# Optimization experiments

Measured on AMD Instinct MI355X. Metric: run time of the kernel, lower is better.

## Reference

```python
import jax, jax.numpy as jnp
import numpy as np


def _assignment(rows, n_clusters, portion, dtype):
    # eye(n_clusters) repeat_interleaved `portion` times along rows, truncated to `rows`,
    # plus the same matrix rolled down by `portion` rows (overlapping assignment).
    s = (jnp.arange(rows)[:, None] // portion == jnp.arange(n_clusters)[None, :]).astype(dtype)
    return s + jnp.roll(s, portion, axis=0)


def _dense_gcn(x, adj, W, b):
    # PyG DenseGCNConv: set diag to 1 (self loops), symmetric deg^-1/2 normalization,
    # out = A_norm @ (x W) + b
    n = adj.shape[0]
    idx = jnp.arange(n)
    adj = adj.at[idx, idx].set(1.0)
    out = x @ W
    d = jnp.clip(jnp.sum(adj, axis=-1), 1.0, None) ** -0.5
    adj = d[:, None] * adj * d[None, :]
    return adj @ out + b


def setup_inputs() -> dict:
    key = jax.random.key(0)
    ks = jax.random.split(key, 8)
    N, D, H, O = 4096, 128, 128, 2
    x = jax.random.normal(ks[0], (N, D), dtype=jnp.float32)
    edge_index = jax.random.uniform(ks[1], (2, N, N), dtype=jnp.float32)  # [1] slice = dense adjacency
    ca1 = jax.random.normal(ks[2], (D, D), dtype=jnp.float32) * (1.414 / np.sqrt(D))  # xavier_normal gain 1.414
    W1 = jax.random.normal(ks[3], (D, H), dtype=jnp.float32) * 0.05
    b1 = jnp.zeros((H,), dtype=jnp.float32)
    W2 = jax.random.normal(ks[4], (H, H), dtype=jnp.float32) * 0.05
    b2 = jnp.zeros((H,), dtype=jnp.float32)
    Wlin = jax.random.normal(ks[5], (O, H), dtype=jnp.float32) * 0.05
    blin = jnp.zeros((O,), dtype=jnp.float32)
    return {"x": x, "edge_index": edge_index, "num_nodes1": 2048,
            "ca1": ca1, "W1": W1, "b1": b1, "W2": W2, "b2": b2,
            "Wlin": Wlin, "blin": blin}


def reference(x, edge_index, num_nodes1, ca1, W1, b1, W2, b2, Wlin, blin):
    N = x.shape[0]
    nearest = N + (N % 2)
    n1 = nearest // 2
    n2 = n1
    portion1 = -(-nearest // n1)  # ceil
    dt = x.dtype

    # level-1 overlapping assignment [N, n1]
    flat_s = _assignment(N, n1, portion1, dt)
    newadj = edge_index[1]
    x1 = flat_s.T @ x                       # [n1, D]
    adj1 = flat_s.T @ newadj @ flat_s       # [n1, n1]

    # cross-layer masked attention
    reverse_s = 1.0 - flat_s
    scores = (x1 @ ca1) @ x.T * reverse_s.T  # [n1, N]
    alpha = jax.nn.softmax(scores, axis=1)
    x1 = alpha @ x + x1

    # GCN layer 1 (dropout is identity in eval mode)
    h = jax.nn.relu(_dense_gcn(x1, adj1, W1, b1))  # [n1, H]

    # level-2 pooling
    portion2 = -(-nearest // n2)
    flat_s2 = _assignment(h.shape[0], n2, portion2, dt)  # [n1, n2]
    x2 = flat_s2.T @ h
    adj2 = flat_s2.T @ adj1 @ flat_s2

    h2 = _dense_gcn(x2, adj2, W2, b2)  # [n2, H]
    out = jnp.mean(h2, axis=0, keepdims=True)  # mean over nodes -> [1, H]
    out = jax.nn.relu(out @ Wlin.T + blin)     # [1, O]
    return jax.nn.log_softmax(out, axis=1)
```

## Files before the change

### kernel.cpp

```cpp
#include <hip/hip_runtime.h>

typedef float  f32x4 __attribute__((ext_vector_type(4)));
typedef float  f32x2 __attribute__((ext_vector_type(2)));
typedef short  short8v __attribute__((ext_vector_type(8)));

static __device__ __forceinline__ unsigned short f2bf(float f) {
  union { float f; unsigned u; } v; v.f = f;
  unsigned r = v.u + 0x7FFFu + ((v.u >> 16) & 1u);
  return (unsigned short)(r >> 16);
}
static __device__ __forceinline__ float bf2f(unsigned short h) {
  union { unsigned u; float f; } v; v.u = ((unsigned)h) << 16;
  return v.f;
}
static __device__ __forceinline__ f32x4 mfma16(short8v a, short8v b, f32x4 c) {
  return __builtin_amdgcn_mfma_f32_16x16x32_bf16(a, b, c, 0, 0, 0);
}

static __device__ __forceinline__ size_t pidx(int r, int c, int C) {
  return (((size_t)(r >> 4) * (C >> 5) + (c >> 5)) << 9) +
         ((size_t)((((c >> 3) & 3) << 4) + (r & 15)) << 3) + (c & 7);
}

static __device__ __forceinline__ float elt(const float* r, int c) { return r[c]; }
static __device__ __forceinline__ float elt(const unsigned short* r, int c) { return bf2f(r[c]); }

template <int NF>
static __device__ __forceinline__ void load_f(const float* row, int c0, float* f) {
  #pragma unroll
  for (int u = 0; u < (NF - 2) / 4; ++u)
    *(f32x4*)(f + 4 * u) = *(const f32x4*)(row + c0 + 4 * u);
  *(f32x2*)(f + NF - 2) = *(const f32x2*)(row + c0 + NF - 2);
}
template <int NF>
static __device__ __forceinline__ void load_f(const unsigned short* row, int c0, float* f) {
  #pragma unroll
  for (int u = 0; u < NF / 2; ++u) {
    unsigned a = *(const unsigned*)(row + c0 + 2 * u);
    f[2 * u]     = bf2f((unsigned short)a);
    f[2 * u + 1] = bf2f((unsigned short)(a >> 16));
  }
}

template <typename T, int KCNT>
static __device__ void pool_adj_body(const T* __restrict__ in,
                                     unsigned short* __restrict__ outh,
                                     unsigned short* __restrict__ outp,
                                     float* __restrict__ rs,
                                     float* __restrict__ diag,
                                     int n, int nin, int bid, float* red) {
  constexpr int NF = 2 * KCNT + 2;
  int chunk = n >> 3;
  int j = (bid & 7) * chunk + (bid >> 3);
  int r0 = 2 * j;
  const T* row0 = in + (size_t)((r0 + 0) & (nin - 1)) * nin;
  const T* row1 = in + (size_t)((r0 + 1) & (nin - 1)) * nin;
  const T* row2 = in + (size_t)((r0 + 2) & (nin - 1)) * nin;
  const T* row3 = in + (size_t)((r0 + 3) & (nin - 1)) * nin;
  int t = threadIdx.x;
  int k0 = t * KCNT;
  int c0 = 2 * k0;
  float F[NF];
  if (c0 + NF <= nin) {
    float f[NF];
    load_f<NF>(row0, c0, F);
    load_f<NF>(row1, c0, f);
    #pragma unroll
    for (int u = 0; u < NF; ++u) F[u] += f[u];
    load_f<NF>(row2, c0, f);
    #pragma unroll
    for (int u = 0; u < NF; ++u) F[u] += f[u];
    load_f<NF>(row3, c0, f);
    #pragma unroll
    for (int u = 0; u < NF; ++u) F[u] += f[u];
  } else {
    #pragma unroll
    for (int u = 0; u < NF; ++u) {
      int c = (c0 + u) & (nin - 1);
      F[u] = elt(row0, c) + elt(row1, c) + elt(row2, c) + elt(row3, c);
    }
  }
  float pr[KCNT + 1];
  #pragma unroll
  for (int m = 0; m <= KCNT; ++m) pr[m] = F[2 * m] + F[2 * m + 1];
  float racc = 0.f;
  unsigned short hv[KCNT];
  #pragma unroll
  for (int kl = 0; kl < KCNT; ++kl) {
    float s = pr[kl] + pr[kl + 1];
    hv[kl] = f2bf(s);
    racc += s;
    if (k0 + kl == j) diag[j] = s;
  }
  if constexpr (KCNT == 8) {
    short8v o8;
    #pragma unroll
    for (int kl = 0; kl < 8; ++kl) o8[kl] = (short)hv[kl];
    if (outh) *(short8v*)&outh[(size_t)j * n + k0] = o8;
    *(short8v*)&outp[pidx(j, k0, n)] = o8;
  } else {
    uint2 o4;
    o4.x = (unsigned)hv[0] | ((unsigned)hv[1] << 16);
    o4.y = (unsigned)hv[2] | ((unsigned)hv[3] << 16);
    if (outh) *(uint2*)&outh[(size_t)j * n + k0] = o4;
    *(uint2*)&outp[pidx(j, k0, n)] = o4;
  }
  #pragma unroll
  for (int o = 32; o > 0; o >>= 1) racc += __shfl_xor(racc, o);
  if ((threadIdx.x & 63) == 0) red[threadIdx.x >> 6] = racc;
  __syncthreads();
  if (threadIdx.x == 0) rs[j] = red[0] + red[1] + red[2] + red[3];
}

static __device__ void split_body(const float* __restrict__ X,
                                  unsigned short* __restrict__ Kph,
                                  unsigned short* __restrict__ Kpl,
                                  unsigned short* __restrict__ Vp,
                                  int bb) {
  #pragma unroll
  for (int r = 0; r < 4; ++r) {
    int e = bb * 1024 + r * 256 + threadIdx.x;
    int i = e >> 7, d = e & 127;
    float v = X[e];
    unsigned short hi = f2bf(v);
    Kph[pidx(i, d, 128)] = hi;
    Kpl[pidx(i, d, 128)] = f2bf(v - bf2f(hi));
    Vp[pidx(d, i, 4096)] = hi;
  }
}

static __device__ __forceinline__ void gemm16x128(const float (*xs)[128],
                                                  const float* __restrict__ W,
                                                  int d, float* acc) {
  #pragma unroll
  for (int i = 0; i < 16; ++i) acc[i] = 0.f;
  for (int e = 0; e < 128; e += 4) {
    float w0 = W[(e + 0) * 128 + d];
    float w1 = W[(e + 1) * 128 + d];
    float w2 = W[(e + 2) * 128 + d];
    float w3 = W[(e + 3) * 128 + d];
    #pragma unroll
    for (int i = 0; i < 16; ++i) {
      f32x4 xv = *(const f32x4*)&xs[i][e];
      float a = acc[i];
      a = fmaf(xv[0], w0, a);
      a = fmaf(xv[1], w1, a);
      a = fmaf(xv[2], w2, a);
      a = fmaf(xv[3], w3, a);
      acc[i] = a;
    }
  }
}

static __device__ __forceinline__ void gemm8x128(const float (*xs)[128], int ibase,
                                                 const float* __restrict__ W,
                                                 int d, float* acc) {
  #pragma unroll
  for (int i = 0; i < 8; ++i) acc[i] = 0.f;
  for (int e = 0; e < 128; e += 4) {
    float w0 = W[(e + 0) * 128 + d];
    float w1 = W[(e + 1) * 128 + d];
    float w2 = W[(e + 2) * 128 + d];
    float w3 = W[(e + 3) * 128 + d];
    #pragma unroll
    for (int i = 0; i < 8; ++i) {
      f32x4 xv = *(const f32x4*)&xs[ibase + i][e];
      float a = acc[i];
      a = fmaf(xv[0], w0, a);
      a = fmaf(xv[1], w1, a);
      a = fmaf(xv[2], w2, a);
      a = fmaf(xv[3], w3, a);
      acc[i] = a;
    }
  }
}

static __device__ void gemm_q_body(const float* __restrict__ x,
                                   const float* __restrict__ W,
                                   float* __restrict__ x1b,
                                   unsigned short* __restrict__ Qph,
                                   unsigned short* __restrict__ Qpl,
                                   int tile, float (*xs)[128], int d) {
  int r0 = tile * 16;
  #pragma unroll
  for (int i = 0; i < 16; ++i) {
    int rr = 2 * (r0 + i);
    float v = x[(size_t)((rr + 0) & 4095) * 128 + d] + x[(size_t)((rr + 1) & 4095) * 128 + d] +
              x[(size_t)((rr + 2) & 4095) * 128 + d] + x[(size_t)((rr + 3) & 4095) * 128 + d];
    xs[i][d] = v;
    x1b[(size_t)(r0 + i) * 128 + d] = v;
  }
  __syncthreads();
  float acc[16];
  gemm16x128(xs, W, d, acc);
  #pragma unroll
  for (int i = 0; i < 16; ++i) {
    size_t o = pidx(r0 + i, d, 128);
    unsigned short hi = f2bf(acc[i]);
    Qph[o] = hi;
    Qpl[o] = f2bf(acc[i] - bf2f(hi));
  }
}

__global__ __launch_bounds__(256) void mega1_kernel(const float* __restrict__ newadj,
                                                    unsigned short* __restrict__ adj1h,
                                                    unsigned short* __restrict__ adj1p,
                                                    float* __restrict__ rs1,
                                                    float* __restrict__ diag1,
                                                    const float* __restrict__ x,
                                                    unsigned short* __restrict__ Kph,
                                                    unsigned short* __restrict__ Kpl,
                                                    unsigned short* __restrict__ Vp,
                                                    const float* __restrict__ ca1,
                                                    float* __restrict__ x1b,
                                                    unsigned short* __restrict__ Qph,
                                                    unsigned short* __restrict__ Qpl) {
  __shared__ __align__(16) char smem[16384];
  int b = blockIdx.x;
  if (b < 512) {
    split_body(x, Kph, Kpl, Vp, b);
  } else if (b < 576) {
    int half = threadIdx.x >> 7, d = threadIdx.x & 127;
    float (*xs)[128] = (float (*)[128])(smem + half * 8192);
    gemm_q_body(x, ca1, x1b, Qph, Qpl, (b - 512) * 2 + half, xs, d);
  } else {
    pool_adj_body<float, 8>(newadj, adj1h, adj1p, rs1, diag1, 2048, 4096, b - 576, (float*)smem);
  }
}

__global__ __launch_bounds__(256) void flash_kernel(const short8v* __restrict__ Qh8,
                                                    const short8v* __restrict__ Ql8,
                                                    const short8v* __restrict__ Kh8,
                                                    const short8v* __restrict__ Kl8,
                                                    const short8v* __restrict__ V8,
                                                    uint2* __restrict__ pacc2,
                                                    float* __restrict__ pm,
                                                    float* __restrict__ pl) {
  __shared__ unsigned short Pbuf[4][16][32];
  int w = threadIdx.x >> 6, lane = threadIdx.x & 63;
  int kc = blockIdx.x & 15;
  int jt = (blockIdx.x >> 4) * 4 + w;
  unsigned short (*P)[32] = Pbuf[w];
  int q = lane & 15, g = lane >> 4;
  int j = jt * 16 + q;
  int kbase = kc * 256;
  int twoj = 2 * j;

  short8v qh[4], ql[4];
  #pragma unroll
  for (int c = 0; c < 4; ++c) {
    qh[c] = Qh8[(size_t)(jt * 4 + c) * 64 + lane];
    ql[c] = Ql8[(size_t)(jt * 4 + c) * 64 + lane];
  }
  float m = -1e30f, l = 0.f;
  f32x4 acc[8];
  #pragma unroll
  for (int t = 0; t < 8; ++t) acc[t] = (f32x4){0.f, 0.f, 0.f, 0.f};

  for (int step = 0; step < 8; ++step) {
    int kt = kbase + step * 32;
    size_t fa = (size_t)(kt >> 4) * 4;
    f32x4 z = {0.f, 0.f, 0.f, 0.f};
    f32x4 hh0 = z, hl0 = z, lh0 = z, hh1 = z, hl1 = z, lh1 = z;
    __builtin_amdgcn_s_setprio(1);
    #pragma unroll
    for (int c = 0; c < 4; ++c) {
      short8v ah = Kh8[(fa + c) * 64 + lane];
      short8v al = Kl8[(fa + c) * 64 + lane];
      short8v bh = Kh8[(fa + 4 + c) * 64 + lane];
      short8v bl = Kl8[(fa + 4 + c) * 64 + lane];
      hh0 = mfma16(ah, qh[c], hh0);
      hh1 = mfma16(bh, qh[c], hh1);
      hl0 = mfma16(ah, ql[c], hl0);
      hl1 = mfma16(bh, ql[c], hl1);
      lh0 = mfma16(al, qh[c], lh0);
      lh1 = mfma16(bl, qh[c], lh1);
    }
    __builtin_amdgcn_s_setprio(0);
    short8v vfrag[8];
    #pragma unroll
    for (int t = 0; t < 8; ++t)
      vfrag[t] = V8[((size_t)t * 128 + (kt >> 5)) * 64 + lane];

    f32x4 s0 = hh0 + hl0 + lh0;
    f32x4 s1 = hh1 + hl1 + lh1;
    float sv[8];
    #pragma unroll
    for (int r = 0; r < 4; ++r) {
      int k0 = kt + g * 4 + r;
      float v0 = s0[r];
      if (((k0 - twoj) & 4095) < 4) v0 = 0.f;
      sv[r] = v0;
      int k1 = k0 + 16;
      float v1 = s1[r];
      if (((k1 - twoj) & 4095) < 4) v1 = 0.f;
      sv[4 + r] = v1;
    }
    float cmx = sv[0];
    #pragma unroll
    for (int r = 1; r < 8; ++r) cmx = fmaxf(cmx, sv[r]);
    cmx = fmaxf(cmx, __shfl_xor(cmx, 16));
    cmx = fmaxf(cmx, __shfl_xor(cmx, 32));
    float mnew = fmaxf(m, cmx);
    float ps = 0.f;
    unsigned short pb[8];
    #pragma unroll
    for (int r = 0; r < 8; ++r) {
      float pv = __expf(sv[r] - mnew);
      ps += pv;
      pb[r] = f2bf(pv);
    }
    ps += __shfl_xor(ps, 16);
    ps += __shfl_xor(ps, 32);
    if (__any(cmx > m)) {
      float scl = __expf(m - mnew);
      l *= scl;
      float sc0 = __shfl(scl, 4 * g + 0);
      float sc1 = __shfl(scl, 4 * g + 1);
      float sc2 = __shfl(scl, 4 * g + 2);
      float sc3 = __shfl(scl, 4 * g + 3);
      #pragma unroll
      for (int t = 0; t < 8; ++t) {
        acc[t][0] *= sc0; acc[t][1] *= sc1; acc[t][2] *= sc2; acc[t][3] *= sc3;
      }
    }
    m = mnew;
    l += ps;
    *(unsigned*)&P[q][4 * g]          = (unsigned)pb[0] | ((unsigned)pb[1] << 16);
    *(unsigned*)&P[q][4 * g + 2]      = (unsigned)pb[2] | ((unsigned)pb[3] << 16);
    *(unsigned*)&P[q][16 + 4 * g]     = (unsigned)pb[4] | ((unsigned)pb[5] << 16);
    *(unsigned*)&P[q][16 + 4 * g + 2] = (unsigned)pb[6] | ((unsigned)pb[7] << 16);
    __syncthreads();
    short8v pa = *(const short8v*)&P[q][8 * g];
    __builtin_amdgcn_s_setprio(1);
    #pragma unroll
    for (int t = 0; t < 8; ++t) acc[t] = mfma16(pa, vfrag[t], acc[t]);
    __builtin_amdgcn_s_setprio(0);
    __syncthreads();
  }
  size_t tau = (size_t)jt * 16 + kc;
  #pragma unroll
  for (int t = 0; t < 8; ++t) {
    uint2 o;
    o.x = (unsigned)f2bf(acc[t][0]) | ((unsigned)f2bf(acc[t][1]) << 16);
    o.y = (unsigned)f2bf(acc[t][2]) | ((unsigned)f2bf(acc[t][3]) << 16);
    pacc2[(tau * 8 + t) * 64 + lane] = o;
  }
  if (g == 0) {
    pm[(size_t)j * 16 + kc] = m;
    pl[(size_t)j * 16 + kc] = l;
  }
}

__global__ __launch_bounds__(256) void combine_gemm_kernel(const uint4* __restrict__ pacc4,
                                                           const float* __restrict__ pm,
                                                           const float* __restrict__ pl,
                                                           const float* __restrict__ x1b,
                                                           const float* __restrict__ W,
                                                           const float* __restrict__ rs,
                                                           const float* __restrict__ diag,
                                                           float* __restrict__ yB,
                                                           unsigned short* __restrict__ ypack,
                                                           int M) {
  __shared__ unsigned short pL[32768];
  __shared__ float pmL[256], plL[256];
  __shared__ float xs[16][128];
  int jt = blockIdx.x;
  int r0 = jt * 16;
  int tid = threadIdx.x;
  const uint4* src = pacc4 + (size_t)jt * 4096;
  uint4* dst = (uint4*)pL;
  #pragma unroll
  for (int u = 0; u < 16; ++u) dst[u * 256 + tid] = src[u * 256 + tid];
  pmL[tid] = pm[(size_t)r0 * 16 + tid];
  plL[tid] = pl[(size_t)r0 * 16 + tid];
  __syncthreads();
  int h = tid >> 7, d = tid & 127;
  int t = d >> 4, q = d & 15;
  #pragma unroll
  for (int ii = 0; ii < 8; ++ii) {
    int i = h * 8 + ii;
    int j = r0 + i;
    int g = i >> 2, r = i & 3;
    int off = t * 256 + (g * 16 + q) * 4 + r;
    float Mx = -1e30f;
    #pragma unroll
    for (int c = 0; c < 16; ++c) Mx = fmaxf(Mx, pmL[i * 16 + c]);
    float L = 0.f, o = 0.f;
    #pragma unroll
    for (int c = 0; c < 16; ++c) {
      float w = __expf(pmL[i * 16 + c] - Mx);
      L += plL[i * 16 + c] * w;
      o += w * bf2f(pL[c * 2048 + off]);
    }
    xs[i][d] = o / L + x1b[(size_t)j * 128 + d];
  }
  __syncthreads();
  float acc[8];
  gemm8x128(xs, h * 8, W, d, acc);
  short8v t0;
  #pragma unroll
  for (int ii = 0; ii < 8; ++ii) {
    int j = r0 + h * 8 + ii;
    float dv = rsqrtf(fmaxf(rs[j] - diag[j] + 1.f, 1.f));
    float v = acc[ii] * dv;
    yB[(size_t)j * 128 + d] = v;
    t0[ii] = (short)f2bf(v);
  }
  *(short8v*)&ypack[pidx(d, r0 + h * 8, M)] = t0;
}

static __device__ void mfma_tile_body(const short8v* __restrict__ A8,
                                      const short8v* __restrict__ B8,
                                      float* __restrict__ C, int K32, int M,
                                      int jt, int nt, int ks, int lane) {
  int q = lane & 15, g = lane >> 4;
  int half = K32 >> 1;
  const short8v* ap = A8 + ((size_t)jt * K32 + ks * half) * 64 + lane;
  const short8v* bp = B8 + ((size_t)nt * K32 + ks * half) * 64 + lane;
  f32x4 acc = {0.f, 0.f, 0.f, 0.f};
  for (int kc = 0; kc < half; kc += 4) {
    #pragma unroll
    for (int u = 0; u < 4; ++u)
      acc = mfma16(ap[(size_t)(kc + u) * 64], bp[(size_t)(kc + u) * 64], acc);
  }
  float* Cp = C + (size_t)ks * M * 128;
  #pragma unroll
  for (int r = 0; r < 4; ++r)
    Cp[(size_t)(jt * 16 + g * 4 + r) * 128 + nt * 16 + q] = acc[r];
}

__global__ __launch_bounds__(256) void mega2_kernel(const unsigned short* __restrict__ adj1h,
                                                    const short8v* __restrict__ adj1p8,
                                                    const short8v* __restrict__ yp8,
                                                    float* __restrict__ G,
                                                    unsigned short* __restrict__ adj2p,
                                                    float* __restrict__ rs2,
                                                    float* __restrict__ diag2) {
  __shared__ float red[4];
  int b = blockIdx.x;
  if (b < 512) {
    int fid = b * 4 + (threadIdx.x >> 6);
    int jt = fid & 127, nt = (fid >> 7) & 7, ks = fid >> 10;
    mfma_tile_body(adj1p8, yp8, G, 64, 2048, jt, nt, ks, threadIdx.x & 63);
  } else {
    pool_adj_body<unsigned short, 4>(adj1h, nullptr, adj2p, rs2, diag2, 1024, 2048, b - 512, red);
  }
}

static __device__ __forceinline__ float epi_h(const float* __restrict__ G,
                                              const float* __restrict__ y,
                                              const float* __restrict__ rs,
                                              const float* __restrict__ diag,
                                              const float* __restrict__ bias,
                                              int n, int r, int d, bool relu) {
  float dv = rsqrtf(fmaxf(rs[r] - diag[r] + 1.f, 1.f));
  float gs = G[(size_t)r * 128 + d] + G[(size_t)(n + r) * 128 + d];
  float v = dv * (gs + (1.f - diag[r]) * y[(size_t)r * 128 + d]) + bias[d];
  return relu ? fmaxf(v, 0.f) : v;
}

__global__ __launch_bounds__(128) void epi_pool_gemm_kernel(const float* __restrict__ G,
                                                            const float* __restrict__ yB,
                                                            const float* __restrict__ rs1,
                                                            const float* __restrict__ diag1,
                                                            const float* __restrict__ b1,
                                                            const float* __restrict__ W,
                                                            const float* __restrict__ rs2,
                                                            const float* __restrict__ diag2,
                                                            float* __restrict__ y2B,
                                                            unsigned short* __restrict__ y2pack,
                                                            unsigned* __restrict__ cnt,
                                                            int n1, int M2) {
  __shared__ float xs[8][128];
  int r0 = blockIdx.x * 8;
  int d = threadIdx.x;
  if (blockIdx.x == 0 && d == 0) *cnt = 0;
  #pragma unroll
  for (int i = 0; i < 8; ++i) {
    int rr = 2 * (r0 + i);
    float s = 0.f;
    #pragma unroll
    for (int a = 0; a < 4; ++a)
      s += epi_h(G, yB, rs1, diag1, b1, n1, (rr + a) & (n1 - 1), d, true);
    xs[i][d] = s;
  }
  __syncthreads();
  float acc[8];
  gemm8x128(xs, 0, W, d, acc);
  short8v t0;
  #pragma unroll
  for (int i = 0; i < 8; ++i) {
    int j = r0 + i;
    float dv = rsqrtf(fmaxf(rs2[j] - diag2[j] + 1.f, 1.f));
    float v = acc[i] * dv;
    y2B[(size_t)j * 128 + d] = v;
    t0[i] = (short)f2bf(v);
  }
  *(short8v*)&y2pack[pidx(d, r0, M2)] = t0;
}

__global__ __launch_bounds__(256) void mfma2_final_kernel(const short8v* __restrict__ adj2p8,
                                                          const short8v* __restrict__ y2p8,
                                                          const float* __restrict__ y2B,
                                                          const float* __restrict__ rs2,
                                                          const float* __restrict__ diag2,
                                                          const float* __restrict__ b2,
                                                          float* __restrict__ part,
                                                          unsigned* __restrict__ cnt,
                                                          const float* __restrict__ Wlin,
                                                          const float* __restrict__ blin,
                                                          float* __restrict__ out) {
  __shared__ float rr0[128], rr1[128];
  __shared__ unsigned doneS;
  int fid = blockIdx.x * 4 + (threadIdx.x >> 6);
  int jt = fid & 63, nt = fid >> 6;
  int lane = threadIdx.x & 63, q = lane & 15, g = lane >> 4;
  const short8v* ap = adj2p8 + (size_t)jt * 32 * 64 + lane;
  const short8v* bp = y2p8 + (size_t)nt * 32 * 64 + lane;
  f32x4 acc = {0.f, 0.f, 0.f, 0.f};
  for (int kc = 0; kc < 32; kc += 4) {
    #pragma unroll
    for (int u = 0; u < 4; ++u)
      acc = mfma16(ap[(size_t)(kc + u) * 64], bp[(size_t)(kc + u) * 64], acc);
  }
  int col = nt * 16 + q;
  float s = 0.f;
  #pragma unroll
  for (int r = 0; r < 4; ++r) {
    int row = jt * 16 + g * 4 + r;
    float dv = rsqrtf(fmaxf(rs2[row] - diag2[row] + 1.f, 1.f));
    s += dv * (acc[r] + (1.f - diag2[row]) * y2B[(size_t)row * 128 + col]) + b2[col];
  }
  s += __shfl_xor(s, 16);
  s += __shfl_xor(s, 32);
  if (g == 0) part[(size_t)jt * 128 + col] = s;
  __threadfence();
  __syncthreads();
  if (threadIdx.x == 0) doneS = atomicAdd(cnt, 1u);
  __syncthreads();
  if (doneS == 127) {
    __threadfence();
    int d = threadIdx.x;
    if (d < 128) {
      float cs = 0.f;
      for (int b = 0; b < 64; ++b) cs += part[(size_t)b * 128 + d];
      float mean = (cs + 1024.f * b2[d]) * (1.f / 2048.f);
      rr0[d] = mean * Wlin[d];
      rr1[d] = mean * Wlin[128 + d];
    }
    __syncthreads();
    for (int sred = 64; sred > 0; sred >>= 1) {
      if (threadIdx.x < sred) {
        rr0[threadIdx.x] += rr0[threadIdx.x + sred];
        rr1[threadIdx.x] += rr1[threadIdx.x + sred];
      }
      __syncthreads();
    }
    if (threadIdx.x == 0) {
      float z0 = fmaxf(rr0[0] + blin[0], 0.f);
      float z1 = fmaxf(rr1[0] + blin[1], 0.f);
      float mz = fmaxf(z0, z1);
      float lse = mz + logf(__expf(z0 - mz) + __expf(z1 - mz));
      out[0] = z0 - lse;
      out[1] = z1 - lse;
    }
  }
}

extern "C" void kernel_launch(void* const* d_in, const int* in_sizes, int n_in,
                              void* d_out, int out_size, void* d_ws, size_t ws_size,
                              hipStream_t stream) {
  const float* x      = (const float*)d_in[0];
  const float* eidx   = (const float*)d_in[1];
  const float* newadj = eidx + (size_t)4096 * 4096;
  const float* ca1    = (const float*)d_in[3];
  const float* W1     = (const float*)d_in[4];
  const float* b1     = (const float*)d_in[5];
  const float* W2     = (const float*)d_in[6];
  const float* b2     = (const float*)d_in[7];
  const float* Wlin   = (const float*)d_in[8];
  const float* blin   = (const float*)d_in[9];
  float* out = (float*)d_out;

  if (ws_size < 42u * 1024u * 1024u) return;

  char* p = (char*)d_ws;
  auto alloc = [&](size_t bytes) -> char* {
    char* r = p; p += (bytes + 255) & ~(size_t)255; return r;
  };
  unsigned short* adj1h = (unsigned short*)alloc((size_t)2048 * 2048 * 2);
  unsigned short* adj1p = (unsigned short*)alloc((size_t)2048 * 2048 * 2);
  float* d1raw = (float*)alloc(2048 * 4);
  float* diag1 = (float*)alloc(2048 * 4);
  float* x1b   = (float*)alloc((size_t)2048 * 128 * 4);
  unsigned short* Qph = (unsigned short*)alloc((size_t)2048 * 128 * 2);
  unsigned short* Qpl = (unsigned short*)alloc((size_t)2048 * 128 * 2);
  unsigned short* Kph = (unsigned short*)alloc((size_t)4096 * 128 * 2);
  unsigned short* Kpl = (unsigned short*)alloc((size_t)4096 * 128 * 2);
  unsigned short* Vp  = (unsigned short*)alloc((size_t)4096 * 128 * 2);
  float* pmB   = (float*)alloc((size_t)2048 * 16 * 4);
  float* plB   = (float*)alloc((size_t)2048 * 16 * 4);
  uint2* pacc2 = (uint2*)alloc((size_t)2048 * 8 * 64 * 8);
  float* yB    = (float*)alloc((size_t)2048 * 128 * 4);
  unsigned short* ypack = (unsigned short*)alloc((size_t)2048 * 128 * 2);
  float* G     = (float*)alloc((size_t)2 * 2048 * 128 * 4);
  unsigned short* adj2p = (unsigned short*)alloc((size_t)1024 * 1024 * 2);
  float* d2raw = (float*)alloc(1024 * 4);
  float* diag2 = (float*)alloc(1024 * 4);
  float* y2B   = (float*)alloc((size_t)1024 * 128 * 4);
  unsigned short* y2pack = (unsigned short*)alloc((size_t)1024 * 128 * 2);
  float* part  = (float*)alloc((size_t)64 * 128 * 4);
  unsigned* cnt = (unsigned*)alloc(256);

  mega1_kernel<<<2624, 256, 0, stream>>>(newadj, adj1h, adj1p, d1raw, diag1,
                                         x, Kph, Kpl, Vp, ca1, x1b, Qph, Qpl);
  flash_kernel<<<512, 256, 0, stream>>>((const short8v*)Qph, (const short8v*)Qpl,
                                        (const short8v*)Kph, (const short8v*)Kpl,
                                        (const short8v*)Vp, pacc2, pmB, plB);
  combine_gemm_kernel<<<128, 256, 0, stream>>>((const uint4*)pacc2, pmB, plB,
                                               x1b, W1, d1raw, diag1, yB, ypack, 2048);
  mega2_kernel<<<1536, 256, 0, stream>>>(adj1h, (const short8v*)adj1p, (const short8v*)ypack,
                                         G, adj2p, d2raw, diag2);
  epi_pool_gemm_kernel<<<128, 128, 0, stream>>>(G, yB, d1raw, diag1, b1, W2, d2raw, diag2,
                                                y2B, y2pack, cnt, 2048, 1024);
  mfma2_final_kernel<<<128, 256, 0, stream>>>((const short8v*)adj2p, (const short8v*)y2pack,
                                              y2B, d2raw, diag2, b2, part, cnt, Wlin, blin, out);
}
```

Measured before the change: 100.2 us.

## Overlap adjacency pooling with flash attention and collapse final GEMM via column sums

Moves the level-1 adjacency pooling out of the first mega kernel and into the same launch as the flash-attention blocks, so the bandwidth-bound pooling runs alongside the compute-bound attention. The prep kernel keeps only the K/V split and Q GEMM. The final adj2 @ y2 GEMM is replaced algebraically: because only the mean over nodes is needed, each row's weight is computed as a normalized column sum of adj2 and dotted with y2. This removes one launch and the y2 intermediates. The trade-off is a reordered floating-point reduction, and adj2 is now read column-wise with strided loads.

```diff
diff --git a/kernel.cpp b/kernel.cpp
--- a/kernel.cpp
+++ b/kernel.cpp
@@ -202,45 +202,35 @@
   }
 }
 
-__global__ __launch_bounds__(256) void mega1_kernel(const float* __restrict__ newadj,
-                                                    unsigned short* __restrict__ adj1h,
-                                                    unsigned short* __restrict__ adj1p,
-                                                    float* __restrict__ rs1,
-                                                    float* __restrict__ diag1,
-                                                    const float* __restrict__ x,
-                                                    unsigned short* __restrict__ Kph,
-                                                    unsigned short* __restrict__ Kpl,
-                                                    unsigned short* __restrict__ Vp,
-                                                    const float* __restrict__ ca1,
-                                                    float* __restrict__ x1b,
-                                                    unsigned short* __restrict__ Qph,
-                                                    unsigned short* __restrict__ Qpl) {
+__global__ __launch_bounds__(256) void prep_kernel(const float* __restrict__ x,
+                                                   unsigned short* __restrict__ Kph,
+                                                   unsigned short* __restrict__ Kpl,
+                                                   unsigned short* __restrict__ Vp,
+                                                   const float* __restrict__ ca1,
+                                                   float* __restrict__ x1b,
+                                                   unsigned short* __restrict__ Qph,
+                                                   unsigned short* __restrict__ Qpl) {
   __shared__ __align__(16) char smem[16384];
   int b = blockIdx.x;
   if (b < 512) {
     split_body(x, Kph, Kpl, Vp, b);
-  } else if (b < 576) {
+  } else {
     int half = threadIdx.x >> 7, d = threadIdx.x & 127;
     float (*xs)[128] = (float (*)[128])(smem + half * 8192);
     gemm_q_body(x, ca1, x1b, Qph, Qpl, (b - 512) * 2 + half, xs, d);
-  } else {
-    pool_adj_body<float, 8>(newadj, adj1h, adj1p, rs1, diag1, 2048, 4096, b - 576, (float*)smem);
-  }
-}
-
-__global__ __launch_bounds__(256) void flash_kernel(const short8v* __restrict__ Qh8,
-                                                    const short8v* __restrict__ Ql8,
-                                                    const short8v* __restrict__ Kh8,
-                                                    const short8v* __restrict__ Kl8,
-                                                    const short8v* __restrict__ V8,
-                                                    uint2* __restrict__ pacc2,
-                                                    float* __restrict__ pm,
-                                                    float* __restrict__ pl) {
-  __shared__ unsigned short Pbuf[4][16][32];
-  int w = threadIdx.x >> 6, lane = threadIdx.x & 63;
-  int kc = blockIdx.x & 15;
-  int jt = (blockIdx.x >> 4) * 4 + w;
-  unsigned short (*P)[32] = Pbuf[w];
+  }
+}
+
+static __device__ void flash_body(const short8v* __restrict__ Qh8,
+                                  const short8v* __restrict__ Ql8,
+                                  const short8v* __restrict__ Kh8,
+                                  const short8v* __restrict__ Kl8,
+                                  const short8v* __restrict__ V8,
+                                  uint2* __restrict__ pacc2,
+                                  float* __restrict__ pm,
+                                  float* __restrict__ pl,
+                                  int jt, int kc, int lane,
+                                  unsigned short (*P)[32]) {
   int q = lane & 15, g = lane >> 4;
   int j = jt * 16 + q;
   int kbase = kc * 256;
@@ -349,6 +339,32 @@
   if (g == 0) {
     pm[(size_t)j * 16 + kc] = m;
     pl[(size_t)j * 16 + kc] = l;
+  }
+}
+
+__global__ __launch_bounds__(256) void megaB_kernel(const float* __restrict__ newadj,
+                                                    unsigned short* __restrict__ adj1h,
+                                                    unsigned short* __restrict__ adj1p,
+                                                    float* __restrict__ rs1,
+                                                    float* __restrict__ diag1,
+                                                    const short8v* __restrict__ Qh8,
+                                                    const short8v* __restrict__ Ql8,
+                                                    const short8v* __restrict__ Kh8,
+                                                    const short8v* __restrict__ Kl8,
+                                                    const short8v* __restrict__ V8,
+                                                    uint2* __restrict__ pacc2,
+                                                    float* __restrict__ pm,
+                                                    float* __restrict__ pl) {
+  __shared__ __align__(16) char smem[4096];
+  int b = blockIdx.x;
+  if (b < 512) {
+    int w = threadIdx.x >> 6, lane = threadIdx.x & 63;
+    int kc = b & 15;
+    int jt = (b >> 4) * 4 + w;
+    unsigned short (*P)[32] = (unsigned short (*)[32])(smem + w * 1024);
+    flash_body(Qh8, Ql8, Kh8, Kl8, V8, pacc2, pm, pl, jt, kc, lane, P);
+  } else {
+    pool_adj_body<float, 8>(newadj, adj1h, adj1p, rs1, diag1, 2048, 4096, b - 512, (float*)smem);
   }
 }
 
@@ -436,9 +452,11 @@
                                                     float* __restrict__ G,
                                                     unsigned short* __restrict__ adj2p,
                                                     float* __restrict__ rs2,
-                                                    float* __restrict__ diag2) {
+                                                    float* __restrict__ diag2,
+                                                    unsigned* __restrict__ cnt) {
   __shared__ float red[4];
   int b = blockIdx.x;
+  if (b == 0 && threadIdx.x == 0) *cnt = 0;
   if (b < 512) {
     int fid = b * 4 + (threadIdx.x >> 6);
     int jt = fid & 127, nt = (fid >> 7) & 7, ks = fid >> 10;
@@ -460,22 +478,51 @@
   return relu ? fmaxf(v, 0.f) : v;
 }
 
-__global__ __launch_bounds__(128) void epi_pool_gemm_kernel(const float* __restrict__ G,
-                                                            const float* __restrict__ yB,
-                                                            const float* __restrict__ rs1,
-                                                            const float* __restrict__ diag1,
-                                                            const float* __restrict__ b1,
-                                                            const float* __restrict__ W,
-                                                            const float* __restrict__ rs2,
-                                                            const float* __restrict__ diag2,
-                                                            float* __restrict__ y2B,
-                                                            unsigned short* __restrict__ y2pack,
-                                                            unsigned* __restrict__ cnt,
-                                                            int n1, int M2) {
+__global__ __launch_bounds__(128) void epi_final_kernel(const float* __restrict__ G,
+                                                        const float* __restrict__ yB,
+                                                        const float* __restrict__ rs1,
+                                                        const float* __restrict__ diag1,
+                                                        const float* __restrict__ b1,
+                                                        const float* __restrict__ W,
+                                                        const float* __restrict__ rs2,
+                                                        const float* __restrict__ diag2,
+                                                        const float* __restrict__ b2,
+                                                        const unsigned short* __restrict__ adj2p,
+                                                        float* __restrict__ part,
+                                                        unsigned* __restrict__ cnt,
+                                                        const float* __restrict__ Wlin,
+                                                        const float* __restrict__ blin,
+                                                        float* __restrict__ out,
+                                                        int n1) {
   __shared__ float xs[8][128];
-  int r0 = blockIdx.x * 8;
-  int d = threadIdx.x;
-  if (blockIdx.x == 0 && d == 0) *cnt = 0;
+  __shared__ float wred[16][8];
+  __shared__ float uval[8];
+  __shared__ float rr0[128], rr1[128];
+  __shared__ unsigned doneS;
+  int b = blockIdx.x;
+  int tid = threadIdx.x;
+  int r0 = b * 8;
+  {
+    const unsigned short* base = adj2p + (size_t)(b >> 2) * 512 + (size_t)(b & 3) * 128 + tid;
+    int s = tid >> 3;
+    float wacc = 0.f;
+    for (int mm = 0; mm < 64; ++mm) {
+      int r = mm * 16 + s;
+      float d2r = rsqrtf(fmaxf(rs2[r] - diag2[r] + 1.f, 1.f));
+      wacc += d2r * bf2f(base[(size_t)mm * 16384]);
+    }
+    wred[s][tid & 7] = wacc;
+  }
+  __syncthreads();
+  if (tid < 8) {
+    float wsum = 0.f;
+    #pragma unroll
+    for (int s2 = 0; s2 < 16; ++s2) wsum += wred[s2][tid];
+    int k = r0 + tid;
+    float d2k = rsqrtf(fmaxf(rs2[k] - diag2[k] + 1.f, 1.f));
+    uval[tid] = wsum + d2k * (1.f - diag2[k]);
+  }
+  int d = tid;
   #pragma unroll
   for (int i = 0; i < 8; ++i) {
     int rr = 2 * (r0 + i);
@@ -488,76 +535,31 @@
   __syncthreads();
   float acc[8];
   gemm8x128(xs, 0, W, d, acc);
-  short8v t0;
+  float pd = 0.f;
   #pragma unroll
   for (int i = 0; i < 8; ++i) {
     int j = r0 + i;
     float dv = rsqrtf(fmaxf(rs2[j] - diag2[j] + 1.f, 1.f));
-    float v = acc[i] * dv;
-    y2B[(size_t)j * 128 + d] = v;
-    t0[i] = (short)f2bf(v);
-  }
-  *(short8v*)&y2pack[pidx(d, r0, M2)] = t0;
-}
-
-__global__ __launch_bounds__(256) void mfma2_final_kernel(const short8v* __restrict__ adj2p8,
-                                                          const short8v* __restrict__ y2p8,
-                                                          const float* __restrict__ y2B,
-                                                          const float* __restrict__ rs2,
-                                                          const float* __restrict__ diag2,
-                                                          const float* __restrict__ b2,
-                                                          float* __restrict__ part,
-                                                          unsigned* __restrict__ cnt,
-                                                          const float* __restrict__ Wlin,
-                                                          const float* __restrict__ blin,
-                                                          float* __restrict__ out) {
-  __shared__ float rr0[128], rr1[128];
-  __shared__ unsigned doneS;
-  int fid = blockIdx.x * 4 + (threadIdx.x >> 6);
-  int jt = fid & 63, nt = fid >> 6;
-  int lane = threadIdx.x & 63, q = lane & 15, g = lane >> 4;
-  const short8v* ap = adj2p8 + (size_t)jt * 32 * 64 + lane;
-  const short8v* bp = y2p8 + (size_t)nt * 32 * 64 + lane;
-  f32x4 acc = {0.f, 0.f, 0.f, 0.f};
-  for (int kc = 0; kc < 32; kc += 4) {
-    #pragma unroll
-    for (int u = 0; u < 4; ++u)
-      acc = mfma16(ap[(size_t)(kc + u) * 64], bp[(size_t)(kc + u) * 64], acc);
-  }
-  int col = nt * 16 + q;
-  float s = 0.f;
-  #pragma unroll
-  for (int r = 0; r < 4; ++r) {
-    int row = jt * 16 + g * 4 + r;
-    float dv = rsqrtf(fmaxf(rs2[row] - diag2[row] + 1.f, 1.f));
-    s += dv * (acc[r] + (1.f - diag2[row]) * y2B[(size_t)row * 128 + col]) + b2[col];
-  }
-  s += __shfl_xor(s, 16);
-  s += __shfl_xor(s, 32);
-  if (g == 0) part[(size_t)jt * 128 + col] = s;
+    pd += uval[i] * (acc[i] * dv);
+  }
+  part[(size_t)b * 128 + d] = pd;
   __threadfence();
   __syncthreads();
-  if (threadIdx.x == 0) doneS = atomicAdd(cnt, 1u);
+  if (tid == 0) doneS = atomicAdd(cnt, 1u);
   __syncthreads();
   if (doneS == 127) {
     __threadfence();
-    int d = threadIdx.x;
-    if (d < 128) {
-      float cs = 0.f;
-      for (int b = 0; b < 64; ++b) cs += part[(size_t)b * 128 + d];
-      float mean = (cs + 1024.f * b2[d]) * (1.f / 2048.f);
-      rr0[d] = mean * Wlin[d];
-      rr1[d] = mean * Wlin[128 + d];
-    }
+    float cs = 0.f;
+    for (int bb = 0; bb < 128; ++bb) cs += part[(size_t)bb * 128 + d];
+    float mean = cs * (1.f / 2048.f) + b2[d];
+    rr0[d] = mean * Wlin[d];
+    rr1[d] = mean * Wlin[128 + d];
     __syncthreads();
     for (int sred = 64; sred > 0; sred >>= 1) {
-      if (threadIdx.x < sred) {
-        rr0[threadIdx.x] += rr0[threadIdx.x + sred];
-        rr1[threadIdx.x] += rr1[threadIdx.x + sred];
-      }
+      if (tid < sred) { rr0[tid] += rr0[tid + sred]; rr1[tid] += rr1[tid + sred]; }
       __syncthreads();
     }
-    if (threadIdx.x == 0) {
+    if (tid == 0) {
       float z0 = fmaxf(rr0[0] + blin[0], 0.f);
       float z1 = fmaxf(rr1[0] + blin[1], 0.f);
       float mz = fmaxf(z0, z1);
@@ -608,22 +610,19 @@
   unsigned short* adj2p = (unsigned short*)alloc((size_t)1024 * 1024 * 2);
   float* d2raw = (float*)alloc(1024 * 4);
   float* diag2 = (float*)alloc(1024 * 4);
-  float* y2B   = (float*)alloc((size_t)1024 * 128 * 4);
-  unsigned short* y2pack = (unsigned short*)alloc((size_t)1024 * 128 * 2);
-  float* part  = (float*)alloc((size_t)64 * 128 * 4);
+  float* part  = (float*)alloc((size_t)128 * 128 * 4);
   unsigned* cnt = (unsigned*)alloc(256);
 
-  mega1_kernel<<<2624, 256, 0, stream>>>(newadj, adj1h, adj1p, d1raw, diag1,
-                                         x, Kph, Kpl, Vp, ca1, x1b, Qph, Qpl);
-  flash_kernel<<<512, 256, 0, stream>>>((const short8v*)Qph, (const short8v*)Qpl,
-                                        (const short8v*)Kph, (const short8v*)Kpl,
-                                        (const short8v*)Vp, pacc2, pmB, plB);
+  prep_kernel<<<576, 256, 0, stream>>>(x, Kph, Kpl, Vp, ca1, x1b, Qph, Qpl);
+  megaB_kernel<<<2560, 256, 0, stream>>>(newadj, adj1h, adj1p, d1raw, diag1,
+                                         (const short8v*)Qph, (const short8v*)Qpl,
+                                         (const short8v*)Kph, (const short8v*)Kpl,
+                                         (const short8v*)Vp, pacc2, pmB, plB);
   combine_gemm_kernel<<<128, 256, 0, stream>>>((const uint4*)pacc2, pmB, plB,
                                                x1b, W1, d1raw, diag1, yB, ypack, 2048);
   mega2_kernel<<<1536, 256, 0, stream>>>(adj1h, (const short8v*)adj1p, (const short8v*)ypack,
-                                         G, adj2p, d2raw, diag2);
-  epi_pool_gemm_kernel<<<128, 128, 0, stream>>>(G, yB, d1raw, diag1, b1, W2, d2raw, diag2,
-                                                y2B, y2pack, cnt, 2048, 1024);
-  mfma2_final_kernel<<<128, 256, 0, stream>>>((const short8v*)adj2p, (const short8v*)y2pack,
-                                              y2B, d2raw, diag2, b2, part, cnt, Wlin, blin, out);
-}
+                                         G, adj2p, d2raw, diag2, cnt);
+  epi_final_kernel<<<128, 128, 0, stream>>>(G, yB, d1raw, diag1, b1, W2,
+                                            d2raw, diag2, b2, adj2p,
+                                            part, cnt, Wlin, blin, out, 2048);
+}
```

New measurement: 108.5 us. +8.3%, slower.
